# Kernel tuning notes

Measured on AMD Instinct MI355X. Metric: run time of the kernel, lower is better.

Reference implementation:

```python
import jax, jax.numpy as jnp
import numpy as np

B, NS, NF, T, D = 64, 2, 13, 24, 512
H = 8
DH = D // H
DFF = 2048
EPS = 1e-5


def setup_inputs() -> dict:
    key = jax.random.key(0)
    ks = jax.random.split(key, 16)
    s = 0.02
    inp = {
        'x': jax.random.normal(ks[0], (B, NS * NF, T, D), jnp.float32),
        'w_in_s': jax.random.normal(ks[1], (3 * D, D), jnp.float32) * s,
        'b_in_s': jnp.zeros((3 * D,), jnp.float32),
        'w_out_s': jax.random.normal(ks[2], (D, D), jnp.float32) * s,
        'b_out_s': jnp.zeros((D,), jnp.float32),
        'w_in_f': jax.random.normal(ks[3], (3 * D, D), jnp.float32) * s,
        'b_in_f': jnp.zeros((3 * D,), jnp.float32),
        'w_out_f': jax.random.normal(ks[4], (D, D), jnp.float32) * s,
        'b_out_f': jnp.zeros((D,), jnp.float32),
        'w1': jax.random.normal(ks[5], (DFF, D), jnp.float32) * s,
        'b1': jnp.zeros((DFF,), jnp.float32),
        'w2': jax.random.normal(ks[6], (D, DFF), jnp.float32) * s,
        'b2': jnp.zeros((D,), jnp.float32),
        'g1': jnp.ones((D,), jnp.float32), 'be1': jnp.zeros((D,), jnp.float32),
        'g2': jnp.ones((D,), jnp.float32), 'be2': jnp.zeros((D,), jnp.float32),
        'g3': jnp.ones((D,), jnp.float32), 'be3': jnp.zeros((D,), jnp.float32),
    }
    return inp


def _layer_norm(x, g, b):
    mu = jnp.mean(x, axis=-1, keepdims=True)
    var = jnp.mean(jnp.square(x - mu), axis=-1, keepdims=True)
    return (x - mu) * jax.lax.rsqrt(var + EPS) * g + b


def _mha(x, w_in, b_in, w_out, b_out):
    # x: [..., S, D]; torch nn.MultiheadAttention math, eval mode (no dropout)
    qkv = x @ w_in.T + b_in                     # [..., S, 3D]
    q, k, v = jnp.split(qkv, 3, axis=-1)
    shp = q.shape[:-1] + (H, DH)
    q, k, v = q.reshape(shp), k.reshape(shp), v.reshape(shp)
    scores = jnp.einsum('...qhd,...khd->...hqk', q, k) / np.sqrt(DH).astype(np.float32)
    a = jax.nn.softmax(scores, axis=-1)
    o = jnp.einsum('...hqk,...khd->...qhd', a, v).reshape(x.shape)
    return o @ w_out.T + b_out


def reference(x, w_in_s, b_in_s, w_out_s, b_out_s, w_in_f, b_in_f, w_out_f, b_out_f,
              w1, b1, w2, b2, g1, be1, g2, be2, g3, be3):
    xr = x.reshape(B, NS, NF, T, D)
    # station attention: attend over the NS axis for each (feature, t)
    xs = xr.transpose(0, 2, 3, 1, 4)            # [B, NF, T, NS, D]
    xs = xs + _mha(xs, w_in_s, b_in_s, w_out_s, b_out_s)
    x = xs.transpose(0, 3, 1, 2, 4).reshape(B, NS * NF, T, D)
    x = _layer_norm(x, g1, be1)
    # feature attention: attend over the NF axis for each (station, t)
    xr = x.reshape(B, NS, NF, T, D)
    xf = xr.transpose(0, 1, 3, 2, 4)            # [B, NS, T, NF, D]
    xf = xf + _mha(xf, w_in_f, b_in_f, w_out_f, b_out_f)
    x = xf.transpose(0, 1, 3, 2, 4).reshape(B, NS * NF, T, D)
    x = _layer_norm(x, g2, be2)
    # feed-forward
    ff = jax.nn.relu(x @ w1.T + b1) @ w2.T + b2
    x = _layer_norm(x + ff, g3, be3)
    return x
```

## Files before the change

kernel.cpp:

```cpp
#include <hip/hip_runtime.h>
#include <stdint.h>

typedef unsigned short u16;
typedef __bf16 bf16x8 __attribute__((ext_vector_type(8)));
typedef float f32x4 __attribute__((ext_vector_type(4)));

#define DEV __device__ __forceinline__

DEV float bf2f(u16 u) {
    union { uint32_t u; float f; } c; c.u = ((uint32_t)u) << 16; return c.f;
}
DEV u16 f2bf(float f) {
    union { float f; uint32_t u; } c; c.f = f;
    uint32_t u = c.u;
    u += 0x7FFFu + ((u >> 16) & 1u);
    return (u16)(u >> 16);
}

DEV void gload_lds16(const u16* gp, u16* lp) {
    __builtin_amdgcn_global_load_lds(
        (__attribute__((address_space(1))) u16*)(uintptr_t)gp,
        (__attribute__((address_space(3))) u16*)lp,
        16, 0, 0);
}

DEV void load16f(const u16* p, float* f) {
    uint4 a = *reinterpret_cast<const uint4*>(p);
    uint4 b = *reinterpret_cast<const uint4*>(p + 8);
    uint32_t w[8] = { a.x, a.y, a.z, a.w, b.x, b.y, b.z, b.w };
#pragma unroll
    for (int k = 0; k < 8; ++k) {
        union { uint32_t u; float f; } lo, hi;
        lo.u = w[k] << 16; hi.u = w[k] & 0xFFFF0000u;
        f[2 * k] = lo.f; f[2 * k + 1] = hi.f;
    }
}
DEV float dot16(const u16* p, const float* q) {
    uint4 a = *reinterpret_cast<const uint4*>(p);
    uint4 b = *reinterpret_cast<const uint4*>(p + 8);
    uint32_t w[8] = { a.x, a.y, a.z, a.w, b.x, b.y, b.z, b.w };
    float d = 0.0f;
#pragma unroll
    for (int k = 0; k < 8; ++k) {
        union { uint32_t u; float f; } lo, hi;
        lo.u = w[k] << 16; hi.u = w[k] & 0xFFFF0000u;
        d += q[2 * k] * lo.f;
        d += q[2 * k + 1] * hi.f;
    }
    return d;
}
DEV void fma16(const u16* p, float pw, float* acc) {
    uint4 a = *reinterpret_cast<const uint4*>(p);
    uint4 b = *reinterpret_cast<const uint4*>(p + 8);
    uint32_t w[8] = { a.x, a.y, a.z, a.w, b.x, b.y, b.z, b.w };
#pragma unroll
    for (int k = 0; k < 8; ++k) {
        union { uint32_t u; float f; } lo, hi;
        lo.u = w[k] << 16; hi.u = w[k] & 0xFFFF0000u;
        acc[2 * k] += pw * lo.f;
        acc[2 * k + 1] += pw * hi.f;
    }
}
DEV void store16(u16* p, const float* y) {
    uint32_t w[8];
#pragma unroll
    for (int k = 0; k < 8; ++k)
        w[k] = (uint32_t)f2bf(y[2 * k]) | ((uint32_t)f2bf(y[2 * k + 1]) << 16);
    uint4 a = { w[0], w[1], w[2], w[3] };
    uint4 b = { w[4], w[5], w[6], w[7] };
    *reinterpret_cast<uint4*>(p) = a;
    *reinterpret_cast<uint4*>(p + 8) = b;
}

__global__ __launch_bounds__(256) void k_f32_to_bf16(
    const float* __restrict__ in, u16* __restrict__ out, int n4)
{
    int i = blockIdx.x * 256 + threadIdx.x;
    if (i >= n4) return;
    float4 v = reinterpret_cast<const float4*>(in)[i];
    ushort4 o;
    o.x = f2bf(v.x); o.y = f2bf(v.y); o.z = f2bf(v.z); o.w = f2bf(v.w);
    reinterpret_cast<ushort4*>(out)[i] = o;
}

template<bool RELU, bool RESID, int NT>
__global__ __launch_bounds__(256) void k_gemm(
    const u16* __restrict__ A, const u16* __restrict__ W,
    const float* __restrict__ bias, const u16* __restrict__ res,
    u16* __restrict__ C, int M, int N, int K)
{
    __shared__ __align__(16) u16 As[2 * 128 * 32];
    __shared__ __align__(16) u16 Bs[2 * 128 * 32];

    const int tid  = threadIdx.x;
    const int lane = tid & 63;
    const int wave = tid >> 6;
    const int wm   = wave >> 1;
    const int wn   = wave & 1;

    const int bid = blockIdx.x;
    const int xcd = bid & 7;
    const int j0  = bid >> 3;
    const long tileM = (long)(xcd * 39 + j0 / NT) * 128;
    const long tileN = (long)(j0 % NT) * 128;

    f32x4 acc[4][4] = {};

    const int r4 = tid >> 2;
    const int c8 = ((tid & 3) ^ ((tid >> 3) & 3)) * 8;
    const u16* Ab = A + (tileM + r4) * (long)K + c8;
    const u16* Wb = W + (tileN + r4) * (long)K + c8;
    const int dst0 = wave * 512;

    const int arow = wm * 64 + (lane & 15);
    const int brow = wn * 64 + (lane & 15);
    const int koff = ((lane >> 4) ^ ((lane >> 1) & 3)) * 8;

    auto stage = [&](int buf, int kk) {
        u16* a0 = As + buf * 4096 + dst0;
        u16* b0 = Bs + buf * 4096 + dst0;
        gload_lds16(Ab + kk,                a0);
        gload_lds16(Ab + kk + (long)64 * K, a0 + 2048);
        gload_lds16(Wb + kk,                b0);
        gload_lds16(Wb + kk + (long)64 * K, b0 + 2048);
    };
    auto compute = [&](int buf) {
        const u16* ab = As + buf * 4096;
        const u16* bb = Bs + buf * 4096;
        bf16x8 a[4], b[4];
#pragma unroll
        for (int f = 0; f < 4; ++f) {
            a[f] = *reinterpret_cast<const bf16x8*>(&ab[(arow + f * 16) * 32 + koff]);
            b[f] = *reinterpret_cast<const bf16x8*>(&bb[(brow + f * 16) * 32 + koff]);
        }
#pragma unroll
        for (int i = 0; i < 4; ++i)
#pragma unroll
            for (int j = 0; j < 4; ++j)
                acc[i][j] = __builtin_amdgcn_mfma_f32_16x16x32_bf16(
                    a[i], b[j], acc[i][j], 0, 0, 0);
    };

    stage(0, 0);
    __syncthreads();

    int cur = 0;
    for (int kk = 0; kk < K - 32; kk += 32) {
        stage(cur ^ 1, kk + 32);
        compute(cur);
        __syncthreads();
        cur ^= 1;
    }
    compute(cur);

    const int crow = (int)tileM + wm * 64 + ((lane >> 4) << 2);
    const int ccol = (int)tileN + wn * 64 + (lane & 15);
#pragma unroll
    for (int i = 0; i < 4; ++i) {
#pragma unroll
        for (int j = 0; j < 4; ++j) {
            const int col = ccol + j * 16;
            const float bv = bias[col];
#pragma unroll
            for (int r = 0; r < 4; ++r) {
                const long row = crow + i * 16 + r;
                float v = acc[i][j][r] + bv;
                if (RESID) v += bf2f(res[row * N + col]);
                if (RELU)  v = fmaxf(v, 0.0f);
                C[row * N + col] = f2bf(v);
            }
        }
    }
}

__global__ __launch_bounds__(256) void k_attn_s(
    const u16* __restrict__ qkv, u16* __restrict__ o)
{
    const int wave = threadIdx.x >> 6, lane = threadIdx.x & 63;
    const int g = blockIdx.x * 4 + wave;
    const int t = g % 24, bf = g / 24, f = bf % 13, b = bf / 13;
    const int base = b * 624 + f * 24 + t;
    const int h = lane >> 3, i = (lane >> 2) & 1, c = lane & 3;
    const int off = h * 64 + c * 16;

    float qf[16];
    load16f(qkv + (size_t)(base + i * 312) * 1536 + off, qf);

    float s[2];
#pragma unroll
    for (int j = 0; j < 2; ++j) {
        float d = dot16(qkv + (size_t)(base + j * 312) * 1536 + 512 + off, qf);
        d += __shfl_xor(d, 1);
        d += __shfl_xor(d, 2);
        s[j] = d * 0.125f;
    }
    const float m = fmaxf(s[0], s[1]);
    const float e0 = expf(s[0] - m), e1 = expf(s[1] - m);
    const float inv = 1.0f / (e0 + e1);
    const float p0 = e0 * inv, p1 = e1 * inv;

    float acc[16] = {};
    fma16(qkv + (size_t)base * 1536 + 1024 + off, p0, acc);
    fma16(qkv + (size_t)(base + 312) * 1536 + 1024 + off, p1, acc);

    store16(o + (size_t)(base + i * 312) * 512 + off, acc);
}

__global__ __launch_bounds__(256) void k_attn_f(
    const u16* __restrict__ qkv, u16* __restrict__ o)
{
    const int wave = threadIdx.x >> 6, lane = threadIdx.x & 63;
    const int p = blockIdx.x * 4 + wave;
    const int h = p & 7, g = p >> 3;
    const int t = g % 24, bs = g / 24, st = bs % 2, b = bs / 2;
    const int base = b * 624 + st * 312 + t;
    const int i = lane >> 2, c = lane & 3;
    const int iq = (i < 13) ? i : 12;
    const int off = h * 64 + c * 16;

    float qf[16];
    load16f(qkv + (size_t)(base + iq * 24) * 1536 + off, qf);

    float sc[13];
#pragma unroll
    for (int j = 0; j < 13; ++j) {
        float d = dot16(qkv + (size_t)(base + j * 24) * 1536 + 512 + off, qf);
        d += __shfl_xor(d, 1);
        d += __shfl_xor(d, 2);
        sc[j] = d * 0.125f;
    }
    float m = sc[0];
#pragma unroll
    for (int j = 1; j < 13; ++j) m = fmaxf(m, sc[j]);
    float den = 0.0f;
#pragma unroll
    for (int j = 0; j < 13; ++j) { sc[j] = expf(sc[j] - m); den += sc[j]; }
    const float inv = 1.0f / den;

    float acc[16] = {};
#pragma unroll
    for (int j = 0; j < 13; ++j)
        fma16(qkv + (size_t)(base + j * 24) * 1536 + 1024 + off, sc[j], acc);
#pragma unroll
    for (int e = 0; e < 16; ++e) acc[e] *= inv;

    if (i < 13)
        store16(o + (size_t)(base + i * 24) * 512 + off, acc);
}

template<bool OUTF32>
__global__ __launch_bounds__(256) void k_ln(
    const u16* __restrict__ in, const float* __restrict__ g,
    const float* __restrict__ be, u16* __restrict__ outb,
    float* __restrict__ outf)
{
    const int row  = blockIdx.x * 4 + (threadIdx.x >> 6);
    const int lane = threadIdx.x & 63;
    const u16* p = in + (size_t)row * 512 + lane * 8;

    uint4 va = *reinterpret_cast<const uint4*>(p);
    uint32_t ua[4] = { va.x, va.y, va.z, va.w };
    float x[8];
#pragma unroll
    for (int i = 0; i < 4; ++i) {
        x[2 * i]     = bf2f((u16)(ua[i] & 0xFFFFu));
        x[2 * i + 1] = bf2f((u16)(ua[i] >> 16));
    }
    float s = 0.f, sq = 0.f;
#pragma unroll
    for (int i = 0; i < 8; ++i) { s += x[i]; sq += x[i] * x[i]; }
#pragma unroll
    for (int off = 32; off; off >>= 1) {
        s  += __shfl_xor(s, off);
        sq += __shfl_xor(sq, off);
    }
    const float mean = s * (1.0f / 512.0f);
    const float var  = sq * (1.0f / 512.0f) - mean * mean;
    const float rstd = rsqrtf(var + 1e-5f);

    const int col = lane * 8;
    float4 g0 = *reinterpret_cast<const float4*>(g + col);
    float4 g1 = *reinterpret_cast<const float4*>(g + col + 4);
    float4 b0 = *reinterpret_cast<const float4*>(be + col);
    float4 b1 = *reinterpret_cast<const float4*>(be + col + 4);
    float gg[8] = { g0.x, g0.y, g0.z, g0.w, g1.x, g1.y, g1.z, g1.w };
    float bb[8] = { b0.x, b0.y, b0.z, b0.w, b1.x, b1.y, b1.z, b1.w };

    float y[8];
#pragma unroll
    for (int i = 0; i < 8; ++i) y[i] = (x[i] - mean) * rstd * gg[i] + bb[i];

    if (OUTF32) {
        float4 o0 = { y[0], y[1], y[2], y[3] };
        float4 o1 = { y[4], y[5], y[6], y[7] };
        reinterpret_cast<float4*>(outf + (size_t)row * 512 + col)[0] = o0;
        reinterpret_cast<float4*>(outf + (size_t)row * 512 + col + 4)[0] = o1;
    } else {
        uint32_t w[4];
#pragma unroll
        for (int i = 0; i < 4; ++i)
            w[i] = (uint32_t)f2bf(y[2 * i]) | ((uint32_t)f2bf(y[2 * i + 1]) << 16);
        uint4 ov = { w[0], w[1], w[2], w[3] };
        *reinterpret_cast<uint4*>(outb + (size_t)row * 512 + col) = ov;
    }
}

extern "C" void kernel_launch(void* const* d_in, const int* in_sizes, int n_in,
                              void* d_out, int out_size, void* d_ws, size_t ws_size,
                              hipStream_t stream)
{
    const float* x       = (const float*)d_in[0];
    const float* w_in_s  = (const float*)d_in[1];
    const float* b_in_s  = (const float*)d_in[2];
    const float* w_out_s = (const float*)d_in[3];
    const float* b_out_s = (const float*)d_in[4];
    const float* w_in_f  = (const float*)d_in[5];
    const float* b_in_f  = (const float*)d_in[6];
    const float* w_out_f = (const float*)d_in[7];
    const float* b_out_f = (const float*)d_in[8];
    const float* w1      = (const float*)d_in[9];
    const float* b1      = (const float*)d_in[10];
    const float* w2      = (const float*)d_in[11];
    const float* b2      = (const float*)d_in[12];
    const float* g1      = (const float*)d_in[13];
    const float* be1     = (const float*)d_in[14];
    const float* g2      = (const float*)d_in[15];
    const float* be2     = (const float*)d_in[16];
    const float* g3      = (const float*)d_in[17];
    const float* be3     = (const float*)d_in[18];

    const int R = 39936;
    u16* xb   = (u16*)d_ws;
    u16* buf1 = xb + (size_t)R * 512;
    u16* obuf = buf1 + (size_t)R * 1536;
    u16* wqs  = buf1 + (size_t)R * 2048;
    u16* wos  = wqs + 1536 * 512;
    u16* wqf  = wos + 512 * 512;
    u16* wof  = wqf + 1536 * 512;
    u16* w1b  = wof + 512 * 512;
    u16* w2b  = w1b + 2048 * 512;

    auto conv = [&](const float* src, u16* dst, int n) {
        int n4 = n / 4;
        k_f32_to_bf16<<<dim3((n4 + 255) / 256), dim3(256), 0, stream>>>(src, dst, n4);
    };
    conv(x,       xb,  R * 512);
    conv(w_in_s,  wqs, 1536 * 512);
    conv(w_out_s, wos, 512 * 512);
    conv(w_in_f,  wqf, 1536 * 512);
    conv(w_out_f, wof, 512 * 512);
    conv(w1,      w1b, 2048 * 512);
    conv(w2,      w2b, 512 * 2048);

    const dim3 blk(256);

    k_gemm<false, false, 12><<<dim3(312 * 12), blk, 0, stream>>>(
        xb, wqs, b_in_s, nullptr, buf1, R, 1536, 512);
    k_attn_s<<<dim3(19968 / 4), blk, 0, stream>>>(buf1, obuf);
    k_gemm<false, true, 4><<<dim3(312 * 4), blk, 0, stream>>>(
        obuf, wos, b_out_s, xb, xb, R, 512, 512);
    k_ln<false><<<dim3(R / 4), blk, 0, stream>>>(xb, g1, be1, xb, nullptr);

    k_gemm<false, false, 12><<<dim3(312 * 12), blk, 0, stream>>>(
        xb, wqf, b_in_f, nullptr, buf1, R, 1536, 512);
    k_attn_f<<<dim3(24576 / 4), blk, 0, stream>>>(buf1, obuf);
    k_gemm<false, true, 4><<<dim3(312 * 4), blk, 0, stream>>>(
        obuf, wof, b_out_f, xb, xb, R, 512, 512);
    k_ln<false><<<dim3(R / 4), blk, 0, stream>>>(xb, g2, be2, xb, nullptr);

    k_gemm<true, false, 16><<<dim3(312 * 16), blk, 0, stream>>>(
        xb, w1b, b1, nullptr, buf1, R, 2048, 512);
    k_gemm<false, true, 4><<<dim3(312 * 4), blk, 0, stream>>>(
        buf1, w2b, b2, xb, xb, R, 512, 2048);
    k_ln<true><<<dim3(R / 4), blk, 0, stream>>>(xb, g3, be3, nullptr, (float*)d_out);
}
```

Baseline: 673.0 us.

## Add 256x256-tile 8-wave pipelined GEMM for QKV and FFN projections

Adds a new 512-thread GEMM kernel that computes 256x256 output tiles with 128-wide K steps. It double-buffers A/B tiles in LDS through direct global-to-LDS loads, interleaving prefetch phases with MFMA phases under explicit vmcnt waits, barriers and setprio. Blocks are remapped in an XCD-aware order so neighbouring tiles land on the same chiplet. The kernel replaces the 128x128 GEMM for the QKV projections and both FFN GEMMs, aiming for more data reuse per tile and better latency hiding. The cost is larger LDS and register use, fewer blocks (only 312 for the FF2 GEMM), and correctness that depends on hand-tuned wait counts.

New measurement: 630.5 us. -6.3%, faster.

```diff
diff --git a/kernel.cpp b/kernel.cpp
--- a/kernel.cpp
+++ b/kernel.cpp
@@ -23,6 +23,10 @@
         (__attribute__((address_space(3))) u16*)lp,
         16, 0, 0);
 }
+
+#define WAITVM4 asm volatile("s_waitcnt vmcnt(4)" ::: "memory")
+#define WAITVM0 asm volatile("s_waitcnt vmcnt(0)" ::: "memory")
+#define MEMFENCE asm volatile("" ::: "memory")
 
 DEV void load16f(const u16* p, float* f) {
     uint4 a = *reinterpret_cast<const uint4*>(p);
@@ -81,6 +85,136 @@
     ushort4 o;
     o.x = f2bf(v.x); o.y = f2bf(v.y); o.z = f2bf(v.z); o.w = f2bf(v.w);
     reinterpret_cast<ushort4*>(out)[i] = o;
+}
+
+template<bool RELU, bool RESID, int NT>
+__global__ __launch_bounds__(512, 2) void k_gemm8p(
+    const u16* __restrict__ A, const u16* __restrict__ W,
+    const float* __restrict__ bias, const u16* __restrict__ res,
+    u16* __restrict__ C, int M, int N, int K)
+{
+    __shared__ __align__(16) u16 Abuf[2][16384];
+    __shared__ __align__(16) u16 Bbuf[2][16384];
+
+    const int tid  = threadIdx.x;
+    const int lane = tid & 63;
+    const int wave = tid >> 6;
+    const int wm   = wave >> 2;
+    const int wn   = wave & 3;
+    const int l15  = lane & 15;
+    const int lg   = lane >> 4;
+
+    const int nwg = gridDim.x;
+    const int v = (blockIdx.x & 7) * (nwg >> 3) + (blockIdx.x >> 3);
+    const long tileM = (long)(v / NT) * 256;
+    const long tileN = (long)(v % NT) * 256;
+
+    const int nIter = K >> 7;
+
+    f32x4 acc[8][4] = {};
+
+    const long Abase = (tileM + (tid >> 3)) * (long)K + (((tid & 7) ^ ((tid >> 3) & 7)) << 3);
+    const long Bbase = (tileN + (tid >> 3)) * (long)K + (((tid & 7) ^ ((tid >> 3) & 7)) << 3);
+
+    auto stA = [&](int h, int t) {
+#pragma unroll
+        for (int e = 0; e < 2; ++e)
+            gload_lds16(A + Abase + (long)(h * 128 + e * 64) * K + t * 64,
+                        &Abuf[t & 1][(h * 1024 + e * 512 + tid) * 8]);
+    };
+    auto stB = [&](int h, int t) {
+#pragma unroll
+        for (int e = 0; e < 2; ++e)
+            gload_lds16(W + Bbase + (long)(h * 128 + e * 64) * K + t * 64,
+                        &Bbuf[t & 1][(h * 1024 + e * 512 + tid) * 8]);
+    };
+
+    int koff[2];
+#pragma unroll
+    for (int ks = 0; ks < 2; ++ks)
+        koff[ks] = ((ks * 4 + lg) ^ (l15 & 7)) * 8;
+    const int aRow = wm * 128 + l15;
+    const int bRow = wn * 64 + l15;
+
+    stA(0, 0); stA(1, 0); stB(0, 0); stB(1, 0); stB(0, 1); stB(1, 1);
+    WAITVM4;
+    MEMFENCE;
+    __builtin_amdgcn_s_barrier();
+    MEMFENCE;
+
+    bf16x8 b[4][2];
+
+    for (int j = 0; j < nIter; ++j) {
+        const bool pre = (j + 1 < nIter);
+        const int E = 2 * j;
+#pragma unroll
+        for (int ph = 0; ph < 8; ++ph) {
+            const int bb = ph >> 2;
+            const int q  = ph & 3;
+            if (q == 0) {
+#pragma unroll
+                for (int n = 0; n < 4; ++n)
+#pragma unroll
+                    for (int ks = 0; ks < 2; ++ks)
+                        b[n][ks] = *reinterpret_cast<const bf16x8*>(
+                            &Bbuf[bb][(bRow + n * 16) * 64 + koff[ks]]);
+            }
+            bf16x8 aq[2][2];
+#pragma unroll
+            for (int mi = 0; mi < 2; ++mi)
+#pragma unroll
+                for (int ks = 0; ks < 2; ++ks)
+                    aq[mi][ks] = *reinterpret_cast<const bf16x8*>(
+                        &Abuf[bb][(aRow + (q * 2 + mi) * 16) * 64 + koff[ks]]);
+            if (ph == 0) stA(0, E + 1);
+            else if (ph == 1) stA(1, E + 1);
+            else if (ph == 2) { if (pre) stB(0, E + 2); }
+            else if (ph == 3) {
+                if (pre) { stB(1, E + 2); WAITVM4; } else { WAITVM0; }
+            }
+            else if (ph == 4) { if (pre) stA(0, E + 2); }
+            else if (ph == 5) { if (pre) stA(1, E + 2); }
+            else if (ph == 6) { if (pre) stB(0, E + 3); }
+            else {
+                if (pre) { stB(1, E + 3); WAITVM4; } else { WAITVM0; }
+            }
+            MEMFENCE;
+            __builtin_amdgcn_s_barrier();
+            MEMFENCE;
+            __builtin_amdgcn_s_setprio(1);
+#pragma unroll
+            for (int mi = 0; mi < 2; ++mi)
+#pragma unroll
+                for (int n = 0; n < 4; ++n)
+#pragma unroll
+                    for (int ks = 0; ks < 2; ++ks)
+                        acc[q * 2 + mi][n] = __builtin_amdgcn_mfma_f32_16x16x32_bf16(
+                            aq[mi][ks], b[n][ks], acc[q * 2 + mi][n], 0, 0, 0);
+            __builtin_amdgcn_s_setprio(0);
+            MEMFENCE;
+            __builtin_amdgcn_s_barrier();
+            MEMFENCE;
+        }
+    }
+
+    const int crow0 = (int)tileM + wm * 128 + ((lane >> 4) << 2);
+    const int ccol0 = (int)tileN + wn * 64 + l15;
+#pragma unroll
+    for (int m = 0; m < 8; ++m) {
+#pragma unroll
+        for (int n = 0; n < 4; ++n) {
+            const int col = ccol0 + n * 16;
+            const float bv = bias[col];
+#pragma unroll
+            for (int r = 0; r < 4; ++r) {
+                const long row = crow0 + m * 16 + r;
+                float vv = acc[m][n][r] + bv;
+                if (RESID) vv += bf2f(res[row * N + col]);
+                if (RELU)  vv = fmaxf(vv, 0.0f);
+                C[row * N + col] = f2bf(vv);
+            }
+        }
+    }
 }
 
 template<bool RELU, bool RESID, int NT>
@@ -352,25 +486,26 @@
     conv(w1,      w1b, 2048 * 512);
     conv(w2,      w2b, 512 * 2048);
 
-    const dim3 blk(256);
-
-    k_gemm<false, false, 12><<<dim3(312 * 12), blk, 0, stream>>>(
+    const dim3 blk256(256);
+    const dim3 blk512(512);
+
+    k_gemm8p<false, false, 6><<<dim3(936), blk512, 0, stream>>>(
         xb, wqs, b_in_s, nullptr, buf1, R, 1536, 512);
-    k_attn_s<<<dim3(19968 / 4), blk, 0, stream>>>(buf1, obuf);
-    k_gemm<false, true, 4><<<dim3(312 * 4), blk, 0, stream>>>(
+    k_attn_s<<<dim3(19968 / 4), blk256, 0, stream>>>(buf1, obuf);
+    k_gemm<false, true, 4><<<dim3(312 * 4), blk256, 0, stream>>>(
         obuf, wos, b_out_s, xb, xb, R, 512, 512);
-    k_ln<false><<<dim3(R / 4), blk, 0, stream>>>(xb, g1, be1, xb, nullptr);
-
-    k_gemm<false, false, 12><<<dim3(312 * 12), blk, 0, stream>>>(
+    k_ln<false><<<dim3(R / 4), blk256, 0, stream>>>(xb, g1, be1, xb, nullptr);
+
+    k_gemm8p<false, false, 6><<<dim3(936), blk512, 0, stream>>>(
         xb, wqf, b_in_f, nullptr, buf1, R, 1536, 512);
-    k_attn_f<<<dim3(24576 / 4), blk, 0, stream>>>(buf1, obuf);
-    k_gemm<false, true, 4><<<dim3(312 * 4), blk, 0, stream>>>(
+    k_attn_f<<<dim3(24576 / 4), blk256, 0, stream>>>(buf1, obuf);
+    k_gemm<false, true, 4><<<dim3(312 * 4), blk256, 0, stream>>>(
         obuf, wof, b_out_f, xb, xb, R, 512, 512);
-    k_ln<false><<<dim3(R / 4), blk, 0, stream>>>(xb, g2, be2, xb, nullptr);
-
-    k_gemm<true, false, 16><<<dim3(312 * 16), blk, 0, stream>>>(
+    k_ln<false><<<dim3(R / 4), blk256, 0, stream>>>(xb, g2, be2, xb, nullptr);
+
+    k_gemm8p<true, false, 8><<<dim3(1248), blk512, 0, stream>>>(
         xb, w1b, b1, nullptr, buf1, R, 2048, 512);
-    k_gemm<false, true, 4><<<dim3(312 * 4), blk, 0, stream>>>(
+    k_gemm8p<false, true, 2><<<dim3(312), blk512, 0, stream>>>(
         buf1, w2b, b2, xb, xb, R, 512, 2048);
-    k_ln<true><<<dim3(R / 4), blk, 0, stream>>>(xb, g3, be3, nullptr, (float*)d_out);
-}
+    k_ln<true><<<dim3(R / 4), blk256, 0, stream>>>(xb, g3, be3, nullptr, (float*)d_out);
+}
```
